# Kernel tuning notes

Measured on AMD Instinct MI355X. Metric: run time of the kernel, lower is better.

The kernel has to match this reference:

```python
import jax, jax.numpy as jnp
import numpy as np

B, H, W, D, C = 2, 128, 128, 8, 64
HEADS, DIM_HEAD = 4, 16
F_IN = C * D            # 512
F_OUT = DIM_HEAD * HEADS * D  # 512


def setup_inputs() -> dict:
    key = jax.random.key(0)
    ks = jax.random.split(key, 8)
    s = 0.02
    return {
        "x_in": jax.random.normal(ks[0], (B, H, W, D, C), dtype=jnp.float32),
        "Wq": jax.random.normal(ks[1], (F_IN, F_OUT), dtype=jnp.float32) * s,
        "Wk": jax.random.normal(ks[2], (F_IN, F_OUT), dtype=jnp.float32) * s,
        "Wv": jax.random.normal(ks[3], (F_IN, F_OUT), dtype=jnp.float32) * s,
        "rescale": jnp.ones((HEADS, 1, 1), dtype=jnp.float32),
        "Wp": jax.random.normal(ks[4], (F_OUT, F_IN), dtype=jnp.float32) * s,
        "bp": jnp.zeros((F_IN,), dtype=jnp.float32),
        "pos_w1": jax.random.normal(ks[5], (C, 1, 3, 3, 3), dtype=jnp.float32) * s,
        "pos_w2": jax.random.normal(ks[6], (C, 1, 3, 3, 3), dtype=jnp.float32) * s,
    }


def _dwconv3d(y, kern, groups):
    # y: [b,c,d,h,w], kern: [c,1,3,3,3] depthwise
    return jax.lax.conv_general_dilated(
        y, kern, window_strides=(1, 1, 1), padding="SAME",
        feature_group_count=groups,
        dimension_numbers=("NCDHW", "OIDHW", "NCDHW"))


def reference(x_in, Wq, Wk, Wv, rescale, Wp, bp, pos_w1, pos_w2):
    b, h, w, d, c = x_in.shape
    heads = rescale.shape[0]
    n = h * w
    x = x_in.reshape(b, n, d * c)
    q_inp = x @ Wq
    k_inp = x @ Wk
    v_inp = x @ Wv

    def split(t):  # [b,n,heads*Dh] -> [b,heads,Dh,n]  (Dh = dim_head*num_frm)
        return t.reshape(b, n, heads, -1).transpose(0, 2, 3, 1)

    q, k, v = split(q_inp), split(k_inp), split(v_inp)
    # L2-normalize along spatial axis n (last dim), torch F.normalize eps=1e-12
    q = q / jnp.maximum(jnp.linalg.norm(q, axis=-1, keepdims=True), 1e-12)
    k = k / jnp.maximum(jnp.linalg.norm(k, axis=-1, keepdims=True), 1e-12)
    # channel attention: [b,heads,Dh,Dh]
    attn = jnp.einsum("bhdn,bhen->bhde", k, q) * rescale
    attn = jax.nn.softmax(attn, axis=-1)
    out = jnp.einsum("bhde,bhen->bhdn", attn, v)  # [b,heads,Dh,n]
    out = out.transpose(0, 3, 1, 2).reshape(b, n, -1)  # [b,n,heads*Dh]
    out_c = (out @ Wp + bp).reshape(b, h, w, d, c)

    # positional branch: depthwise conv3d over [b,c,d,h,w]
    vp = v_inp.reshape(b, h, w, d, c).transpose(0, 4, 3, 1, 2)
    p = _dwconv3d(vp, pos_w1, c)
    p = jax.nn.gelu(p, approximate=False)
    p = _dwconv3d(p, pos_w2, c)
    out_p = p.transpose(0, 3, 4, 2, 1)  # -> [b,h,w,d,c]
    return out_c + out_p
```

## Files before the change

kernel.cpp:

```cpp
#include <hip/hip_runtime.h>
#include <math.h>
#include <stdint.h>


using short8  = __attribute__((ext_vector_type(8))) short;
using f32x4   = __attribute__((ext_vector_type(4))) float;

__device__ __forceinline__ float bf2f(unsigned short u) {
  union { unsigned int i; float f; } v; v.i = ((unsigned int)u) << 16; return v.f;
}
__device__ __forceinline__ unsigned short f2bf(float f) {
  union { float f; unsigned int i; } v; v.f = f;
  unsigned int r = v.i + 0x7fffu + ((v.i >> 16) & 1u);
  return (unsigned short)(r >> 16);
}

__device__ __forceinline__ void g2l16(const void* g, void* l) {
  __builtin_amdgcn_global_load_lds(
      (__attribute__((address_space(1))) void*)(unsigned long long)(uintptr_t)g,
      (__attribute__((address_space(3))) void*)(unsigned int)(uintptr_t)l,
      16, 0, 0);
}

__global__ __launch_bounds__(256) void convert_x(const float* __restrict__ x,
                                                 unsigned short* __restrict__ xb) {
  int i = (blockIdx.x * 256 + threadIdx.x) * 4;
  float4 v = *(const float4*)&x[i];
  ushort4 o;
  o.x = f2bf(v.x); o.y = f2bf(v.y); o.z = f2bf(v.z); o.w = f2bf(v.w);
  *(ushort4*)&xb[i] = o;
}

__global__ __launch_bounds__(256) void prep_w(const float* __restrict__ Wq,
                                              const float* __restrict__ Wk,
                                              const float* __restrict__ Wv,
                                              const float* __restrict__ Wp,
                                              unsigned short* __restrict__ Wcat_t,
                                              unsigned short* __restrict__ Wp_t) {
  __shared__ unsigned short Ls[32 * 36];
  int bid = blockIdx.x;
  int mat = bid >> 8, tile = bid & 255;
  int tr = (tile >> 4) * 32, tc = (tile & 15) * 32;
  const float* src = (mat == 0) ? Wq : (mat == 1) ? Wk : (mat == 2) ? Wv : Wp;
  int t = threadIdx.x;
  int r = t >> 3, c4 = (t & 7) * 4;
  float4 v = *(const float4*)&src[(tr + r) * 512 + tc + c4];
  Ls[(c4 + 0) * 36 + r] = f2bf(v.x);
  Ls[(c4 + 1) * 36 + r] = f2bf(v.y);
  Ls[(c4 + 2) * 36 + r] = f2bf(v.z);
  Ls[(c4 + 3) * 36 + r] = f2bf(v.w);
  __syncthreads();
  int rn = t >> 3, ck4 = (t & 7) * 4;
  ushort4 o;
  o.x = Ls[rn * 36 + ck4 + 0]; o.y = Ls[rn * 36 + ck4 + 1];
  o.z = Ls[rn * 36 + ck4 + 2]; o.w = Ls[rn * 36 + ck4 + 3];
  unsigned short* dst = (mat < 3)
      ? &Wcat_t[(long)(mat * 512 + tc + rn) * 512 + tr + ck4]
      : &Wp_t[(long)(tc + rn) * 512 + tr + ck4];
  *(ushort4*)dst = o;
}

__global__ __launch_bounds__(256, 2) void fused_qkv(
    const unsigned short* __restrict__ x_bf,
    const unsigned short* __restrict__ Wcat_t,
    unsigned short* __restrict__ v,
    float* __restrict__ Gp, float* __restrict__ ss) {
  __shared__ unsigned short sh[38912];
  unsigned short* As = sh;
  unsigned short* B0 = sh + 8192;
  unsigned short* B1 = sh + 16384;
  const int job = blockIdx.x, mt = blockIdx.y, b = blockIdx.z;
  const int t = threadIdx.x;
  const int lane = t & 63, w = t >> 6;
  const int wm = w >> 1, wn = w & 1;
  const int quad = lane >> 4, l16 = lane & 15;
  const int sr = lane >> 3, sc = lane & 7;
  const unsigned short* A = x_bf + ((long)b * 16384 + mt * 128) * 512;

  if (job >= 4) {
    const unsigned short* Bt = Wcat_t + (long)(1024 + (job - 4) * 128) * 512;
    f32x4 acc[4][4] = {};
    for (int k0 = 0; k0 < 512; k0 += 64) {
#pragma unroll
      for (int q = 0; q < 4; q++) {
        int r = q * 32 + w * 8 + sr;
        int ca = (sc ^ sr) * 8;
        g2l16(&A[(long)r * 512 + k0 + ca], &As[(q * 32 + w * 8) * 64]);
        g2l16(&Bt[(long)r * 512 + k0 + ca], &B0[(q * 32 + w * 8) * 64]);
      }
      __syncthreads();
#pragma unroll
      for (int kk = 0; kk < 2; kk++) {
        short8 af[4], bf[4];
#pragma unroll
        for (int i = 0; i < 4; i++) {
          int r = wm * 64 + i * 16 + l16;
          int s = (kk * 4 + quad) ^ (r & 7);
          af[i] = *(const short8*)&As[r * 64 + s * 8];
        }
#pragma unroll
        for (int j = 0; j < 4; j++) {
          int r = wn * 64 + j * 16 + l16;
          int s = (kk * 4 + quad) ^ (r & 7);
          bf[j] = *(const short8*)&B0[r * 64 + s * 8];
        }
#pragma unroll
        for (int i = 0; i < 4; i++)
#pragma unroll
          for (int j = 0; j < 4; j++)
            acc[i][j] = __builtin_amdgcn_mfma_f32_16x16x32_bf16(bf[j], af[i], acc[i][j], 0, 0, 0);
      }
      __syncthreads();
    }
    unsigned short* vout = v + ((long)b * 16384 + mt * 128) * 512 + (job - 4) * 128;
#pragma unroll
    for (int i = 0; i < 4; i++) {
      long rbase = (long)(wm * 64 + i * 16 + l16) * 512;
#pragma unroll
      for (int j = 0; j < 4; j++) {
        int col = wn * 64 + j * 16 + quad * 4;
        uint2 o;
        o.x = (unsigned)f2bf(acc[i][j][0]) | ((unsigned)f2bf(acc[i][j][1]) << 16);
        o.y = (unsigned)f2bf(acc[i][j][2]) | ((unsigned)f2bf(acc[i][j][3]) << 16);
        *(uint2*)&vout[rbase + col] = o;
      }
    }
  } else {
    const int h = job;
    const unsigned short* Bq = Wcat_t + (long)(h * 128) * 512;
    const unsigned short* Bk = Wcat_t + (long)(512 + h * 128) * 512;
    f32x4 aq[4][4] = {}, ak[4][4] = {};
    for (int k0 = 0; k0 < 512; k0 += 64) {
#pragma unroll
      for (int q = 0; q < 4; q++) {
        int r = q * 32 + w * 8 + sr;
        int ca = (sc ^ sr) * 8;
        g2l16(&A[(long)r * 512 + k0 + ca],  &As[(q * 32 + w * 8) * 64]);
        g2l16(&Bq[(long)r * 512 + k0 + ca], &B0[(q * 32 + w * 8) * 64]);
        g2l16(&Bk[(long)r * 512 + k0 + ca], &B1[(q * 32 + w * 8) * 64]);
      }
      __syncthreads();
#pragma unroll
      for (int kk = 0; kk < 2; kk++) {
        short8 af[4], bq[4], bk[4];
#pragma unroll
        for (int i = 0; i < 4; i++) {
          int r = wm * 64 + i * 16 + l16;
          int s = (kk * 4 + quad) ^ (r & 7);
          af[i] = *(const short8*)&As[r * 64 + s * 8];
        }
#pragma unroll
        for (int j = 0; j < 4; j++) {
          int r = wn * 64 + j * 16 + l16;
          int s = (kk * 4 + quad) ^ (r & 7);
          bq[j] = *(const short8*)&B0[r * 64 + s * 8];
          bk[j] = *(const short8*)&B1[r * 64 + s * 8];
        }
#pragma unroll
        for (int i = 0; i < 4; i++)
#pragma unroll
          for (int j = 0; j < 4; j++) {
            aq[i][j] = __builtin_amdgcn_mfma_f32_16x16x32_bf16(af[i], bq[j], aq[i][j], 0, 0, 0);
            ak[i][j] = __builtin_amdgcn_mfma_f32_16x16x32_bf16(af[i], bk[j], ak[i][j], 0, 0, 0);
          }
      }
      __syncthreads();
    }
    unsigned short* kT = sh;
    unsigned short* qT = sh + 17408;
    float* red = (float*)(sh + 34816);
#pragma unroll
    for (int i = 0; i < 4; i++) {
      int mm = wm * 64 + i * 16 + quad * 4;
#pragma unroll
      for (int j = 0; j < 4; j++) {
        int f = wn * 64 + j * 16 + l16;
        ushort4 oq = { f2bf(aq[i][j][0]), f2bf(aq[i][j][1]), f2bf(aq[i][j][2]), f2bf(aq[i][j][3]) };
        ushort4 ok = { f2bf(ak[i][j][0]), f2bf(ak[i][j][1]), f2bf(ak[i][j][2]), f2bf(ak[i][j][3]) };
        *(ushort4*)&qT[f * 136 + mm] = oq;
        *(ushort4*)&kT[f * 136 + mm] = ok;
      }
    }
    int grp = wm * 4 + quad;
#pragma unroll
    for (int j = 0; j < 4; j++) {
      float pq = 0.f, pk = 0.f;
#pragma unroll
      for (int i = 0; i < 4; i++)
#pragma unroll
        for (int r = 0; r < 4; r++) { pq += aq[i][j][r] * aq[i][j][r]; pk += ak[i][j][r] * ak[i][j][r]; }
      int col = wn * 64 + j * 16 + l16;
      red[grp * 128 + col] = pq;
      red[1024 + grp * 128 + col] = pk;
    }
    __syncthreads();
    f32x4 g[4][4] = {};
#pragma unroll
    for (int kk2 = 0; kk2 < 4; kk2++) {
      short8 afk[4], bfq[4];
#pragma unroll
      for (int i = 0; i < 4; i++)
        afk[i] = *(const short8*)&kT[(wm * 64 + i * 16 + l16) * 136 + kk2 * 32 + quad * 8];
#pragma unroll
      for (int j = 0; j < 4; j++)
        bfq[j] = *(const short8*)&qT[(wn * 64 + j * 16 + l16) * 136 + kk2 * 32 + quad * 8];
#pragma unroll
      for (int i = 0; i < 4; i++)
#pragma unroll
        for (int j = 0; j < 4; j++)
          g[i][j] = __builtin_amdgcn_mfma_f32_16x16x32_bf16(afk[i], bfq[j], g[i][j], 0, 0, 0);
    }
    float* gp = Gp + (((long)(b * 128 + mt) * 4 + h) << 14);
#pragma unroll
    for (int i = 0; i < 4; i++) {
      int dd = wm * 64 + i * 16 + quad * 4;
#pragma unroll
      for (int j = 0; j < 4; j++) {
        int e = wn * 64 + j * 16 + l16;
        *(f32x4*)&gp[e * 128 + dd] = g[i][j];
      }
    }
    {
      int sel = t >> 7, col = t & 127;
      float s = 0.f;
#pragma unroll
      for (int g2 = 0; g2 < 8; g2++) s += red[sel * 1024 + g2 * 128 + col];
      atomicAdd(&ss[b * 1024 + sel * 512 + h * 128 + col], s);
    }
  }
}

__global__ __launch_bounds__(256) void reduce_g(const float* __restrict__ Gp,
                                                float* __restrict__ G) {
  int i = blockIdx.x * 256 + threadIdx.x;
  int b = i >> 16, h = (i >> 14) & 3, r = i & 16383;
  const float* p = Gp + (((long)b * 512 + h) << 14) + r;
  float s = 0.f;
#pragma unroll 8
  for (int mtv = 0; mtv < 128; mtv++) s += p[(long)mtv * 65536];
  G[i] = s;
}

__global__ __launch_bounds__(256) void softmax_kernel(const float* __restrict__ Gt,
                                                      const float* __restrict__ ss,
                                                      const float* __restrict__ rescale,
                                                      unsigned short* __restrict__ Abd) {
  __shared__ float L[128 * 129];
  __shared__ float rsq[128];
  __shared__ float rsk[128];
  int h = blockIdx.x, b = blockIdx.y;
  int t = threadIdx.x;
  const float* g = Gt + (long)(b * 4 + h) * 16384;
  if (t < 128) rsq[t] = rsqrtf(fmaxf(ss[b * 1024 + h * 128 + t], 1e-24f));
  else { int d = t - 128; rsk[d] = rsqrtf(fmaxf(ss[b * 1024 + 512 + h * 128 + d], 1e-24f)); }
  __syncthreads();
  float rs = rescale[h];
  for (int i = t; i < 16384; i += 256) {
    int e = i >> 7, d = i & 127;
    L[d * 129 + e] = g[i] * rsk[d] * rsq[e] * rs;
  }
  __syncthreads();
  if (t < 128) {
    float* row = &L[t * 129];
    float mx = -1e30f;
    for (int e = 0; e < 128; e++) mx = fmaxf(mx, row[e]);
    float sum = 0.0f;
    for (int e = 0; e < 128; e++) { float ex = __expf(row[e] - mx); row[e] = ex; sum += ex; }
    float inv = 1.0f / sum;
    long abase = (long)b * 262144;
    for (int e = 0; e < 128; e++)
      Abd[abase + (long)(h * 128 + e) * 512 + h * 128 + t] = f2bf(row[e] * inv);
  }
}

__global__ __launch_bounds__(256) void gemm_lds(
    const unsigned short* __restrict__ A, const unsigned short* __restrict__ Bt,
    unsigned short* __restrict__ C, const float* __restrict__ bias,
    int lda, int ldb, int ldc, int K, long sA, long sB, long sC) {
  __shared__ unsigned short As[128 * 64];
  __shared__ unsigned short Bs[128 * 64];
  const int t = threadIdx.x;
  const int n0 = blockIdx.x * 128, m0 = blockIdx.y * 128;
  A  += (long)blockIdx.z * sA + (long)m0 * lda;
  Bt += (long)blockIdx.z * sB + (long)n0 * ldb;
  C  += (long)blockIdx.z * sC;
  const int lane = t & 63, w = t >> 6;
  const int wm = w >> 1, wn = w & 1;
  const int quad = lane >> 4, l16 = lane & 15;
  const int sr = lane >> 3, sc = lane & 7;

  f32x4 acc[4][4] = {};

  for (int k0 = 0; k0 < K; k0 += 64) {
#pragma unroll
    for (int q = 0; q < 4; q++) {
      int r = q * 32 + w * 8 + sr;
      int ca = (sc ^ sr) * 8;
      g2l16(&A[(long)r * lda + k0 + ca], &As[(q * 32 + w * 8) * 64]);
      g2l16(&Bt[(long)r * ldb + k0 + ca], &Bs[(q * 32 + w * 8) * 64]);
    }
    __syncthreads();
#pragma unroll
    for (int kk = 0; kk < 2; kk++) {
      short8 af[4], bfq[4];
#pragma unroll
      for (int i = 0; i < 4; i++) {
        int r = wm * 64 + i * 16 + l16;
        int s = (kk * 4 + quad) ^ (r & 7);
        af[i] = *(const short8*)&As[r * 64 + s * 8];
      }
#pragma unroll
      for (int j = 0; j < 4; j++) {
        int r = wn * 64 + j * 16 + l16;
        int s = (kk * 4 + quad) ^ (r & 7);
        bfq[j] = *(const short8*)&Bs[r * 64 + s * 8];
      }
#pragma unroll
      for (int i = 0; i < 4; i++)
#pragma unroll
        for (int j = 0; j < 4; j++)
          acc[i][j] = __builtin_amdgcn_mfma_f32_16x16x32_bf16(bfq[j], af[i], acc[i][j], 0, 0, 0);
    }
    __syncthreads();
  }

#pragma unroll
  for (int i = 0; i < 4; i++) {
    long rbase = (long)(m0 + wm * 64 + i * 16 + l16) * ldc;
#pragma unroll
    for (int j = 0; j < 4; j++) {
      int col = n0 + wn * 64 + j * 16 + quad * 4;
      float b0 = 0.f, b1 = 0.f, b2 = 0.f, b3 = 0.f;
      if (bias) { float4 bv = *(const float4*)&bias[col]; b0 = bv.x; b1 = bv.y; b2 = bv.z; b3 = bv.w; }
      uint2 o;
      o.x = (unsigned)f2bf(acc[i][j][0] + b0) | ((unsigned)f2bf(acc[i][j][1] + b1) << 16);
      o.y = (unsigned)f2bf(acc[i][j][2] + b2) | ((unsigned)f2bf(acc[i][j][3] + b3) << 16);
      *(uint2*)&C[rbase + col] = o;
    }
  }
}

template <bool GELU>
__global__ __launch_bounds__(256) void dwconv_kernel(
    const unsigned short* __restrict__ in,
    const float* __restrict__ wgt,
    const unsigned short* __restrict__ addc,
    unsigned short* __restrict__ outb,
    float* __restrict__ outf) {
  __shared__ unsigned short tile[60 * 512];
  __shared__ float wl[27 * 64];
  int wt = blockIdx.x, ht = blockIdx.y, b = blockIdx.z;
  int t = threadIdx.x;
  for (int i = t; i < 1728; i += 256) {
    int c = i / 27, tap = i % 27;
    wl[tap * 64 + c] = wgt[i];
  }
  int h0 = ht * 4, w0 = wt * 8;
  int lg = t & 63;
#pragma unroll 5
  for (int rr = 0; rr < 15; rr++) {
    int row = rr * 4 + (t >> 6);
    int hh = row / 10, ww = row % 10;
    int gh = h0 + hh - 1, gw = w0 + ww - 1;
    uint4 vv = {0u, 0u, 0u, 0u};
    if ((unsigned)gh < 128u && (unsigned)gw < 128u)
      vv = *(const uint4*)&in[((long)(b * 16384 + gh * 128 + gw)) * 512 + lg * 8];
    *(uint4*)&tile[row * 512 + lg * 8] = vv;
  }
  __syncthreads();

  int f0 = lg * 8;
  int d = f0 >> 6, c0 = f0 & 63;
  int pg = t >> 6;
  int pwb = (pg & 1) * 4;
#pragma unroll
  for (int P = 0; P < 2; P++) {
    int ph = P * 2 + (pg >> 1);
    float acc[4][8] = {};
    for (int kd = 0; kd < 3; kd++) {
      int dz = d + kd - 1;
      if ((unsigned)dz >= 8u) continue;
      int fz = dz * 64 + c0;
#pragma unroll
      for (int kh = 0; kh < 3; kh++) {
        float tf[6][8];
#pragma unroll
        for (int cc = 0; cc < 6; cc++) {
          uint4 pv = *(const uint4*)&tile[((ph + kh) * 10 + pwb + cc) * 512 + fz];
          const unsigned short* u = (const unsigned short*)&pv;
#pragma unroll
          for (int j = 0; j < 8; j++) tf[cc][j] = bf2f(u[j]);
        }
#pragma unroll
        for (int kw = 0; kw < 3; kw++) {
          int tap = kd * 9 + kh * 3 + kw;
          float wv[8];
          *(float4*)&wv[0] = *(const float4*)&wl[tap * 64 + c0];
          *(float4*)&wv[4] = *(const float4*)&wl[tap * 64 + c0 + 4];
#pragma unroll
          for (int s = 0; s < 4; s++)
#pragma unroll
            for (int j = 0; j < 8; j++) acc[s][j] += tf[s + kw][j] * wv[j];
        }
      }
    }
#pragma unroll
    for (int s = 0; s < 4; s++) {
      int pw = pwb + s;
      long row = (long)(b * 16384 + (h0 + ph) * 128 + (w0 + pw));
      if (GELU) {
        unsigned short o[8];
#pragma unroll
        for (int j = 0; j < 8; j++) {
          float xg = acc[s][j];
          o[j] = f2bf(0.5f * xg * (1.0f + erff(xg * 0.70710678118654752f)));
        }
        *(uint4*)&outb[row * 512 + f0] = *(uint4*)&o[0];
      } else {
        uint4 av = *(const uint4*)&addc[row * 512 + f0];
        const unsigned short* au = (const unsigned short*)&av;
        float o[8];
#pragma unroll
        for (int j = 0; j < 8; j++) o[j] = acc[s][j] + bf2f(au[j]);
        *(float4*)&outf[row * 512 + f0]     = *(float4*)&o[0];
        *(float4*)&outf[row * 512 + f0 + 4] = *(float4*)&o[4];
      }
    }
  }
}

extern "C" void kernel_launch(void* const* d_in, const int* in_sizes, int n_in,
                              void* d_out, int out_size, void* d_ws, size_t ws_size,
                              hipStream_t stream) {
  const float* x   = (const float*)d_in[0];
  const float* Wq  = (const float*)d_in[1];
  const float* Wk  = (const float*)d_in[2];
  const float* Wv  = (const float*)d_in[3];
  const float* rsc = (const float*)d_in[4];
  const float* Wp  = (const float*)d_in[5];
  const float* bp  = (const float*)d_in[6];
  const float* pw1 = (const float*)d_in[7];
  const float* pw2 = (const float*)d_in[8];
  float* out = (float*)d_out;

  char* ws = (char*)d_ws;
  unsigned short* x_bf   = (unsigned short*)(ws + 0);
  unsigned short* v      = (unsigned short*)(ws + 33554432);
  unsigned short* out_c  = (unsigned short*)(ws + 67108864);
  float*          Gp     = (float*)(ws + 100663296);
  unsigned short* Wcat_t = (unsigned short*)(ws + 167772160);
  unsigned short* Wp_t   = (unsigned short*)(ws + 169345024);
  float*          ss     = (float*)(ws + 169869312);
  float*          G      = (float*)(ws + 169877504);
  unsigned short* Abd    = (unsigned short*)(ws + 170401792);
  unsigned short* Mt     = (unsigned short*)(ws + 171450368);
  unsigned short* p1     = x_bf;

  hipMemsetAsync(ss, 0, 8192, stream);
  hipMemsetAsync(Abd, 0, 1048576, stream);

  convert_x<<<16384, 256, 0, stream>>>(x, x_bf);
  prep_w<<<1024, 256, 0, stream>>>(Wq, Wk, Wv, Wp, Wcat_t, Wp_t);

  fused_qkv<<<dim3(8, 128, 2), 256, 0, stream>>>(x_bf, Wcat_t, v, Gp, ss);
  reduce_g<<<512, 256, 0, stream>>>(Gp, G);
  softmax_kernel<<<dim3(4, 2, 1), 256, 0, stream>>>(G, ss, rsc, Abd);

  gemm_lds<<<dim3(4, 4, 2), 256, 0, stream>>>(
      Wp_t, Abd, Mt, nullptr, 512, 512, 512, 512, 0L, 262144L, 262144L);

  gemm_lds<<<dim3(4, 128, 2), 256, 0, stream>>>(
      v, Mt, out_c, bp, 512, 512, 512, 512,
      (long)16384 * 512, 262144L, (long)16384 * 512);

  dwconv_kernel<true><<<dim3(16, 32, 2), 256, 0, stream>>>(
      v, pw1, nullptr, p1, nullptr);
  dwconv_kernel<false><<<dim3(16, 32, 2), 256, 0, stream>>>(
      p1, pw2, out_c, nullptr, out);
}
```

Baseline: 373.2 us.

## Split fused QKV kernel into Q/K Gram and V GEMM kernels

```diff
diff --git a/kernel.cpp b/kernel.cpp
--- a/kernel.cpp
+++ b/kernel.cpp
@@ -60,75 +60,27 @@
   *(ushort4*)dst = o;
 }
 
-__global__ __launch_bounds__(256, 2) void fused_qkv(
+__global__ __launch_bounds__(256, 2) void qk_gram(
     const unsigned short* __restrict__ x_bf,
     const unsigned short* __restrict__ Wcat_t,
-    unsigned short* __restrict__ v,
     float* __restrict__ Gp, float* __restrict__ ss) {
   __shared__ unsigned short sh[38912];
   unsigned short* As = sh;
   unsigned short* B0 = sh + 8192;
   unsigned short* B1 = sh + 16384;
-  const int job = blockIdx.x, mt = blockIdx.y, b = blockIdx.z;
+  const int mt2 = blockIdx.x, h = blockIdx.y, b = blockIdx.z;
   const int t = threadIdx.x;
   const int lane = t & 63, w = t >> 6;
   const int wm = w >> 1, wn = w & 1;
   const int quad = lane >> 4, l16 = lane & 15;
   const int sr = lane >> 3, sc = lane & 7;
-  const unsigned short* A = x_bf + ((long)b * 16384 + mt * 128) * 512;
-
-  if (job >= 4) {
-    const unsigned short* Bt = Wcat_t + (long)(1024 + (job - 4) * 128) * 512;
-    f32x4 acc[4][4] = {};
-    for (int k0 = 0; k0 < 512; k0 += 64) {
-#pragma unroll
-      for (int q = 0; q < 4; q++) {
-        int r = q * 32 + w * 8 + sr;
-        int ca = (sc ^ sr) * 8;
-        g2l16(&A[(long)r * 512 + k0 + ca], &As[(q * 32 + w * 8) * 64]);
-        g2l16(&Bt[(long)r * 512 + k0 + ca], &B0[(q * 32 + w * 8) * 64]);
-      }
-      __syncthreads();
-#pragma unroll
-      for (int kk = 0; kk < 2; kk++) {
-        short8 af[4], bf[4];
-#pragma unroll
-        for (int i = 0; i < 4; i++) {
-          int r = wm * 64 + i * 16 + l16;
-          int s = (kk * 4 + quad) ^ (r & 7);
-          af[i] = *(const short8*)&As[r * 64 + s * 8];
-        }
-#pragma unroll
-        for (int j = 0; j < 4; j++) {
-          int r = wn * 64 + j * 16 + l16;
-          int s = (kk * 4 + quad) ^ (r & 7);
-          bf[j] = *(const short8*)&B0[r * 64 + s * 8];
-        }
-#pragma unroll
-        for (int i = 0; i < 4; i++)
-#pragma unroll
-          for (int j = 0; j < 4; j++)
-            acc[i][j] = __builtin_amdgcn_mfma_f32_16x16x32_bf16(bf[j], af[i], acc[i][j], 0, 0, 0);
-      }
-      __syncthreads();
-    }
-    unsigned short* vout = v + ((long)b * 16384 + mt * 128) * 512 + (job - 4) * 128;
-#pragma unroll
-    for (int i = 0; i < 4; i++) {
-      long rbase = (long)(wm * 64 + i * 16 + l16) * 512;
-#pragma unroll
-      for (int j = 0; j < 4; j++) {
-        int col = wn * 64 + j * 16 + quad * 4;
-        uint2 o;
-        o.x = (unsigned)f2bf(acc[i][j][0]) | ((unsigned)f2bf(acc[i][j][1]) << 16);
-        o.y = (unsigned)f2bf(acc[i][j][2]) | ((unsigned)f2bf(acc[i][j][3]) << 16);
-        *(uint2*)&vout[rbase + col] = o;
-      }
-    }
-  } else {
-    const int h = job;
-    const unsigned short* Bq = Wcat_t + (long)(h * 128) * 512;
-    const unsigned short* Bk = Wcat_t + (long)(512 + h * 128) * 512;
+  const unsigned short* Bq = Wcat_t + (long)(h * 128) * 512;
+  const unsigned short* Bk = Wcat_t + (long)(512 + h * 128) * 512;
+
+  f32x4 g[4][4] = {};
+
+  for (int half = 0; half < 2; half++) {
+    const unsigned short* A = x_bf + ((long)b * 16384 + (mt2 * 2 + half) * 128) * 512;
     f32x4 aq[4][4] = {}, ak[4][4] = {};
     for (int k0 = 0; k0 < 512; k0 += 64) {
 #pragma unroll
@@ -194,7 +146,6 @@
       red[1024 + grp * 128 + col] = pk;
     }
     __syncthreads();
-    f32x4 g[4][4] = {};
 #pragma unroll
     for (int kk2 = 0; kk2 < 4; kk2++) {
       short8 afk[4], bfq[4];
@@ -209,16 +160,6 @@
 #pragma unroll
         for (int j = 0; j < 4; j++)
           g[i][j] = __builtin_amdgcn_mfma_f32_16x16x32_bf16(afk[i], bfq[j], g[i][j], 0, 0, 0);
-    }
-    float* gp = Gp + (((long)(b * 128 + mt) * 4 + h) << 14);
-#pragma unroll
-    for (int i = 0; i < 4; i++) {
-      int dd = wm * 64 + i * 16 + quad * 4;
-#pragma unroll
-      for (int j = 0; j < 4; j++) {
-        int e = wn * 64 + j * 16 + l16;
-        *(f32x4*)&gp[e * 128 + dd] = g[i][j];
-      }
     }
     {
       int sel = t >> 7, col = t & 127;
@@ -226,6 +167,81 @@
 #pragma unroll
       for (int g2 = 0; g2 < 8; g2++) s += red[sel * 1024 + g2 * 128 + col];
       atomicAdd(&ss[b * 1024 + sel * 512 + h * 128 + col], s);
+    }
+    __syncthreads();
+  }
+
+  float* gp = Gp + (((long)(b * 64 + mt2) * 4 + h) << 14);
+#pragma unroll
+  for (int i = 0; i < 4; i++) {
+    int dd = wm * 64 + i * 16 + quad * 4;
+#pragma unroll
+    for (int j = 0; j < 4; j++) {
+      int e = wn * 64 + j * 16 + l16;
+      *(f32x4*)&gp[e * 128 + dd] = g[i][j];
+    }
+  }
+}
+
+__global__ __launch_bounds__(256, 3) void v_gemm(
+    const unsigned short* __restrict__ x_bf,
+    const unsigned short* __restrict__ Wcat_t,
+    unsigned short* __restrict__ v) {
+  __shared__ unsigned short As[8192];
+  __shared__ unsigned short Bs[8192];
+  const int mt = blockIdx.x, nt = blockIdx.y, b = blockIdx.z;
+  const int t = threadIdx.x;
+  const int lane = t & 63, w = t >> 6;
+  const int wm = w >> 1, wn = w & 1;
+  const int quad = lane >> 4, l16 = lane & 15;
+  const int sr = lane >> 3, sc = lane & 7;
+  const unsigned short* A  = x_bf + ((long)b * 16384 + mt * 128) * 512;
+  const unsigned short* Bt = Wcat_t + (long)(1024 + nt * 128) * 512;
+
+  f32x4 acc[4][4] = {};
+  for (int k0 = 0; k0 < 512; k0 += 64) {
+#pragma unroll
+    for (int q = 0; q < 4; q++) {
+      int r = q * 32 + w * 8 + sr;
+      int ca = (sc ^ sr) * 8;
+      g2l16(&A[(long)r * 512 + k0 + ca],  &As[(q * 32 + w * 8) * 64]);
+      g2l16(&Bt[(long)r * 512 + k0 + ca], &Bs[(q * 32 + w * 8) * 64]);
+    }
+    __syncthreads();
+#pragma unroll
+    for (int kk = 0; kk < 2; kk++) {
+      short8 af[4], bf[4];
+#pragma unroll
+      for (int i = 0; i < 4; i++) {
+        int r = wm * 64 + i * 16 + l16;
+        int s = (kk * 4 + quad) ^ (r & 7);
+        af[i] = *(const short8*)&As[r * 64 + s * 8];
+      }
+#pragma unroll
+      for (int j = 0; j < 4; j++) {
+        int r = wn * 64 + j * 16 + l16;
+        int s = (kk * 4 + quad) ^ (r & 7);
+        bf[j] = *(const short8*)&Bs[r * 64 + s * 8];
+      }
+#pragma unroll
+      for (int i = 0; i < 4; i++)
+#pragma unroll
+        for (int j = 0; j < 4; j++)
+          acc[i][j] = __builtin_amdgcn_mfma_f32_16x16x32_bf16(bf[j], af[i], acc[i][j], 0, 0, 0);
+    }
+    __syncthreads();
+  }
+  unsigned short* vout = v + ((long)b * 16384 + mt * 128) * 512 + nt * 128;
+#pragma unroll
+  for (int i = 0; i < 4; i++) {
+    long rbase = (long)(wm * 64 + i * 16 + l16) * 512;
+#pragma unroll
+    for (int j = 0; j < 4; j++) {
+      int col = wn * 64 + j * 16 + quad * 4;
+      uint2 o;
+      o.x = (unsigned)f2bf(acc[i][j][0]) | ((unsigned)f2bf(acc[i][j][1]) << 16);
+      o.y = (unsigned)f2bf(acc[i][j][2]) | ((unsigned)f2bf(acc[i][j][3]) << 16);
+      *(uint2*)&vout[rbase + col] = o;
     }
   }
 }
@@ -234,10 +250,10 @@
                                                 float* __restrict__ G) {
   int i = blockIdx.x * 256 + threadIdx.x;
   int b = i >> 16, h = (i >> 14) & 3, r = i & 16383;
-  const float* p = Gp + (((long)b * 512 + h) << 14) + r;
+  const float* p = Gp + (((long)b * 256 + h) << 14) + r;
   float s = 0.f;
 #pragma unroll 8
-  for (int mtv = 0; mtv < 128; mtv++) s += p[(long)mtv * 65536];
+  for (int mtv = 0; mtv < 64; mtv++) s += p[(long)mtv * 65536];
   G[i] = s;
 }
 
@@ -273,14 +289,14 @@
   }
 }
 
-__global__ __launch_bounds__(256) void gemm_lds(
+__global__ __launch_bounds__(256, 3) void gemm_lds(
     const unsigned short* __restrict__ A, const unsigned short* __restrict__ Bt,
     unsigned short* __restrict__ C, const float* __restrict__ bias,
     int lda, int ldb, int ldc, int K, long sA, long sB, long sC) {
   __shared__ unsigned short As[128 * 64];
   __shared__ unsigned short Bs[128 * 64];
   const int t = threadIdx.x;
-  const int n0 = blockIdx.x * 128, m0 = blockIdx.y * 128;
+  const int m0 = blockIdx.x * 128, n0 = blockIdx.y * 128;
   A  += (long)blockIdx.z * sA + (long)m0 * lda;
   Bt += (long)blockIdx.z * sB + (long)n0 * ldb;
   C  += (long)blockIdx.z * sC;
@@ -462,14 +478,16 @@
   convert_x<<<16384, 256, 0, stream>>>(x, x_bf);
   prep_w<<<1024, 256, 0, stream>>>(Wq, Wk, Wv, Wp, Wcat_t, Wp_t);
 
-  fused_qkv<<<dim3(8, 128, 2), 256, 0, stream>>>(x_bf, Wcat_t, v, Gp, ss);
+  qk_gram<<<dim3(64, 4, 2), 256, 0, stream>>>(x_bf, Wcat_t, Gp, ss);
+  v_gemm<<<dim3(128, 4, 2), 256, 0, stream>>>(x_bf, Wcat_t, v);
+
   reduce_g<<<512, 256, 0, stream>>>(Gp, G);
   softmax_kernel<<<dim3(4, 2, 1), 256, 0, stream>>>(G, ss, rsc, Abd);
 
   gemm_lds<<<dim3(4, 4, 2), 256, 0, stream>>>(
       Wp_t, Abd, Mt, nullptr, 512, 512, 512, 512, 0L, 262144L, 262144L);
 
-  gemm_lds<<<dim3(4, 128, 2), 256, 0, stream>>>(
+  gemm_lds<<<dim3(128, 4, 2), 256, 0, stream>>>(
       v, Mt, out_c, bp, 512, 512, 512, 512,
       (long)16384 * 512, 262144L, (long)16384 * 512);
 
```

New measurement: 351.8 us. 1.06x faster.
